# Kernel tuning notes

Measured on AMD Instinct MI355X. Metric: run time of the kernel, lower is better.

## Reference

```python
import jax, jax.numpy as jnp
import numpy as np

IN_DIM, INTER, OUT, CLS = 512, 128, 64, 4
MID, BOT = 1600, 6400
N = 1 + MID + BOT
E = 160000


def setup_inputs() -> dict:
    key = jax.random.key(0)
    ki = iter(jax.random.split(key, 48))

    def nrm(shape, s=0.02):
        return jax.random.normal(next(ki), shape, dtype=jnp.float32) * s

    z = lambda *s: jnp.zeros(s, jnp.float32)
    inp = {}
    inp["x"] = jax.random.normal(next(ki), (N, IN_DIM), dtype=jnp.float32)
    inp["edge_index"] = jax.random.randint(next(ki), (2, E), 0, N)
    # PatchRelevance 1 (in=512 -> 128)
    inp["Wq1"], inp["bq1"] = nrm((IN_DIM, INTER)), z(INTER)
    inp["Wk1"], inp["bk1"] = nrm((IN_DIM, INTER)), z(INTER)
    inp["Wv1"], inp["bv1"] = nrm((IN_DIM, INTER)), z(INTER)
    # PatchRelevance 2 (128 -> 64)
    inp["Wq2"], inp["bq2"] = nrm((INTER, OUT)), z(OUT)
    inp["Wk2"], inp["bk2"] = nrm((INTER, OUT)), z(OUT)
    inp["Wv2"], inp["bv2"] = nrm((INTER, OUT)), z(OUT)
    # GCN convs
    inp["Wg1"], inp["bg1"] = nrm((IN_DIM, INTER)), z(INTER)
    inp["Wg2"], inp["bg2"] = nrm((INTER, OUT)), z(OUT)
    # squeeze MLPs
    inp["Ws1"], inp["bs1"] = nrm((2 * INTER, INTER)), z(INTER)
    inp["Ws2"], inp["bs2"] = nrm((2 * OUT, OUT)), z(OUT)
    # heads
    inp["Wfc1"], inp["bfc1"] = nrm((3 * OUT, OUT)), z(OUT)
    inp["Wfc2"], inp["bfc2"] = nrm((OUT, CLS)), z(CLS)
    inp["Wtw"], inp["btw"] = nrm((OUT, CLS)), z(CLS)
    inp["Wmid"], inp["bmid"] = nrm((OUT, CLS)), z(CLS)
    inp["Wbot"], inp["bbot"] = nrm((OUT, CLS)), z(CLS)
    # sparse_attention Conv1d(out_dim -> 4, k=4, s=4)  weight layout OIH
    inp["Wconv"] = nrm((4, OUT, 4))
    inp["bconv"] = z(4)
    inp["arch0"] = MID
    inp["arch1"] = BOT
    return inp


def _patch_rel(x, Wq, bq, Wk, bk, Wv, bv):
    q = x @ Wq + bq
    k = x @ Wk + bk
    v = x @ Wv + bv
    att = jax.nn.softmax(q @ k.T, axis=-1)  # [N, N]
    return att @ v


def _gcn(x, src, dst, W, b, n):
    # PyG GCNConv: add self-loops (already in src/dst), symmetric deg^-1/2 norm
    deg = jax.ops.segment_sum(jnp.ones_like(src, dtype=x.dtype), dst, num_segments=n)
    dinv = jnp.where(deg > 0, jax.lax.rsqrt(deg), 0.0)
    norm = dinv[src] * dinv[dst]
    h = x @ W
    out = jax.ops.segment_sum(h[src] * norm[:, None], dst, num_segments=n)
    return out + b


def reference(x, edge_index, Wq1, bq1, Wk1, bk1, Wv1, bv1, Wq2, bq2, Wk2, bk2,
              Wv2, bv2, Wg1, bg1, Wg2, bg2, Ws1, bs1, Ws2, bs2, Wfc1, bfc1,
              Wfc2, bfc2, Wtw, btw, Wmid, bmid, Wbot, bbot, Wconv, bconv,
              arch0, arch1):
    n = x.shape[0]
    loop = jnp.arange(n, dtype=edge_index.dtype)
    src = jnp.concatenate([edge_index[0], loop])
    dst = jnp.concatenate([edge_index[1], loop])

    r1 = _patch_rel(x, Wq1, bq1, Wk1, bk1, Wv1, bv1)
    g1 = _gcn(x, src, dst, Wg1, bg1, n)
    s1 = jax.nn.relu(jax.nn.relu(jnp.concatenate([g1, r1], axis=1)) @ Ws1 + bs1)

    r2 = _patch_rel(s1, Wq2, bq2, Wk2, bk2, Wv2, bv2)
    g2 = _gcn(s1, src, dst, Wg2, bg2, n)
    s2 = jax.nn.relu(jax.nn.relu(jnp.concatenate([g2, r2], axis=1)) @ Ws2 + bs2)

    tw = s2[0:1]                                   # [1, OUT]
    mid_features = s2[1:1 + arch0]                 # [arch0, OUT]
    mid_avg = jnp.mean(mid_features, axis=0, keepdims=True)
    bf = s2[1 + arch0:1 + arch0 + arch1]           # [arch1, OUT]

    # Conv1d(OUT -> 4, k=4, s=4) over node axis: [1, OUT, arch1] -> [1, 4, arch0]
    bw = jax.lax.conv_general_dilated(bf.T[None], Wconv, (4,), 'VALID',
                                      dimension_numbers=('NCH', 'OIH', 'NCH'))[0]
    bw = bw + bconv[:, None]                       # [4, arch0]
    # index_copy_ with strided indices == interleave channels: wv[i*4+j] = bw[j, i]
    wv = bw.T.reshape(-1)
    wv = wv / jnp.max(wv)
    grp = wv.reshape(arch0, 4)
    grp = grp / jnp.sum(jnp.abs(grp), axis=-1, keepdims=True)
    wv = grp.reshape(arch1, 1)

    tree_bottom = ((wv * bf).T.reshape(-1, arch0, 4).sum(-1)).T  # [arch0, OUT]
    bottom_weighted = (jnp.sum(wv * bf, axis=0) / arch0).reshape(1, -1)

    out_tw = tw @ Wtw + btw
    out_mid = mid_avg @ Wmid + bmid
    out_bottom = bottom_weighted @ Wbot + bbot
    gcn_feat = jnp.concatenate([tw, mid_avg, bottom_weighted], axis=-1) @ Wfc1 + bfc1
    out_gcn = jax.nn.relu(gcn_feat) @ Wfc2 + bfc2
    return (out_gcn, out_tw, out_mid, out_bottom, gcn_feat, tw, mid_avg,
            bottom_weighted, wv, mid_features, tree_bottom)
```

## Files before the change

### kernel.cpp

```cpp
#include <hip/hip_runtime.h>
#include <math.h>

#define N_NODES 8001
#define NPAD    8032
#define E_EDGES 160000
#define NQTOT   8064
#define LOG2E   1.4426950408889634f
#define NSPLIT  16

typedef unsigned short u16;
typedef __attribute__((ext_vector_type(8)))  short bf16x8;
typedef __attribute__((ext_vector_type(16))) float f32x16;

__device__ __forceinline__ short f2bf(float f) {
    unsigned u = __builtin_bit_cast(unsigned, f);
    u = (u + 0x7FFFu + ((u >> 16) & 1u)) >> 16;
    return (short)u;
}
__device__ __forceinline__ float bf2f(u16 x) {
    return __builtin_bit_cast(float, (unsigned)x << 16);
}
__device__ __forceinline__ int pk2(float a, float b) {
    int r;
    asm("v_cvt_pk_bf16_f32 %0, %1, %2" : "=v"(r) : "v"(a), "v"(b));
    return r;
}

#define GLDS(g, l) __builtin_amdgcn_global_load_lds( \
    (const __attribute__((address_space(1))) void*)(g), \
    (__attribute__((address_space(3))) void*)(l), 16, 0, 0)

template<int K>
__global__ __launch_bounds__(256) void cast_rows(const float* __restrict__ A,
                                                 u16* __restrict__ B)
{
    size_t t = (size_t)blockIdx.x * 256 + threadIdx.x;
    int row = (int)(t / (K / 8));
    int c8  = (int)(t % (K / 8)) * 8;
    int lrow = min(row, N_NODES - 1);
    const float4* p = (const float4*)&A[(size_t)lrow * K + c8];
    float4 u = p[0], v = p[1];
    int4 w = { pk2(u.x, u.y), pk2(u.z, u.w), pk2(v.x, v.y), pk2(v.z, v.w) };
    *(int4*)&B[t * 8] = w;
}

__global__ __launch_bounds__(256) void wtrans_all(
    const float* __restrict__ Wq1, const float* __restrict__ Wk1,
    const float* __restrict__ Wv1, const float* __restrict__ Wg1,
    const float* __restrict__ Wq2, const float* __restrict__ Wk2,
    const float* __restrict__ Wv2, const float* __restrict__ Wg2,
    const float* __restrict__ Ws1, const float* __restrict__ Ws2,
    u16* __restrict__ WT1, u16* __restrict__ WT2,
    u16* __restrict__ WST1, u16* __restrict__ WST2)
{
    const int b = blockIdx.x, tid = threadIdx.x;
    if (b < 1024) {
        int t = b * 256 + tid;
        int p = t / (128 * 512), n = (t / 512) & 127, k = t % 512;
        const float* W = (p == 0) ? Wq1 : (p == 1) ? Wk1 : (p == 2) ? Wv1 : Wg1;
        float v = W[k * 128 + n];
        if (p == 0) v *= LOG2E;
        WT1[t] = (u16)f2bf(v);
    } else if (b < 1152) {
        int t = (b - 1024) * 256 + tid;
        int p = t / (64 * 128), n = (t / 128) & 63, k = t & 127;
        const float* W = (p == 0) ? Wq2 : (p == 1) ? Wk2 : (p == 2) ? Wv2 : Wg2;
        float v = W[k * 64 + n];
        if (p == 0) v *= LOG2E;
        WT2[t] = (u16)f2bf(v);
    } else if (b < 1280) {
        int t = (b - 1152) * 256 + tid;
        int n = t >> 8, k = t & 255;
        WST1[t] = (u16)f2bf(Ws1[k * 128 + n]);
    } else {
        int t = (b - 1280) * 256 + tid;
        int n = t >> 7, k = t & 127;
        WST2[t] = (u16)f2bf(Ws2[k * 64 + n]);
    }
}

template<int K, int MOUT>
__global__ __launch_bounds__(256) void proj4_mfma(
    const u16* __restrict__ Xb, const u16* __restrict__ WT,
    const float* __restrict__ bq, const float* __restrict__ bk,
    const float* __restrict__ bv,
    u16* __restrict__ Qb, u16* __restrict__ Kb, u16* __restrict__ VTb,
    float* __restrict__ Hb)
{
    constexpr int NKC  = K / 16;
    constexpr int NNT  = MOUT / 32;
    constexpr int ROWB = K / 8;
    constexpr int NB   = 32 * ROWB;

    __shared__ u16 xs[32 * K];

    const int tid = threadIdx.x, wid = tid >> 6, lane = tid & 63;
    const int q = lane & 31, gp = lane >> 5;
    const int m0 = blockIdx.x * 32;

    for (int i = tid; i < NB; i += 256) {
        int row = i / ROWB, blk = i % ROWB;
        GLDS(&Xb[(size_t)(m0 + row) * K + 8 * (blk ^ (row & 7))], &xs[i * 8]);
    }
    __syncthreads();

    f32x16 acc[NNT];
#pragma unroll
    for (int nt = 0; nt < NNT; nt++) acc[nt] = f32x16{};

    const u16* wbase = WT + (size_t)wid * MOUT * K;

#pragma unroll 4
    for (int c = 0; c < NKC; c++) {
        bf16x8 af = *(const bf16x8*)&xs[q * K + 8 * ((2 * c + gp) ^ (q & 7))];
#pragma unroll
        for (int nt = 0; nt < NNT; nt++) {
            bf16x8 bf = *(const bf16x8*)&wbase[(size_t)(nt * 32 + q) * K + 16 * c + 8 * gp];
            acc[nt] = __builtin_amdgcn_mfma_f32_32x32x16_bf16(af, bf, acc[nt], 0, 0, 0);
        }
    }

    if (wid == 0) {
#pragma unroll
        for (int nt = 0; nt < NNT; nt++) {
            float bb = bq[nt * 32 + q] * LOG2E;
#pragma unroll
            for (int r = 0; r < 16; r++) {
                int grow = m0 + (r & 3) + 8 * (r >> 2) + 4 * gp;
                Qb[(size_t)grow * MOUT + nt * 32 + q] = (u16)f2bf(acc[nt][r] + bb);
            }
        }
    } else if (wid == 1) {
#pragma unroll
        for (int nt = 0; nt < NNT; nt++) {
            float bb = bk[nt * 32 + q];
#pragma unroll
            for (int r = 0; r < 16; r++) {
                int grow = m0 + (r & 3) + 8 * (r >> 2) + 4 * gp;
                Kb[(size_t)grow * MOUT + nt * 32 + q] = (u16)f2bf(acc[nt][r] + bb);
            }
        }
    } else if (wid == 2) {
#pragma unroll
        for (int nt = 0; nt < NNT; nt++) {
            float bb = bv[nt * 32 + q];
            u16* vrow = &VTb[(size_t)(nt * 32 + q) * NPAD];
#pragma unroll
            for (int g = 0; g < 4; g++) {
                ushort4 s;
                s.x = (u16)f2bf(acc[nt][4 * g + 0] + bb);
                s.y = (u16)f2bf(acc[nt][4 * g + 1] + bb);
                s.z = (u16)f2bf(acc[nt][4 * g + 2] + bb);
                s.w = (u16)f2bf(acc[nt][4 * g + 3] + bb);
                *(ushort4*)&vrow[m0 + 8 * g + 4 * gp] = s;
            }
        }
    } else {
#pragma unroll
        for (int nt = 0; nt < NNT; nt++) {
#pragma unroll
            for (int r = 0; r < 16; r++) {
                int grow = m0 + (r & 3) + 8 * (r >> 2) + 4 * gp;
                if (grow < N_NODES)
                    Hb[(size_t)grow * MOUT + nt * 32 + q] = acc[nt][r];
            }
        }
    }
}

template<int K, int MOUT, int OM, int NW>
__global__ __launch_bounds__(NW * 64) void s_gemm_mfma(
    const u16* __restrict__ Ab, const u16* __restrict__ WT,
    const float* __restrict__ bias, void* __restrict__ Cv)
{
    constexpr int NKC  = K / 16;
    constexpr int ROWB = K / 8;
    constexpr int NB   = 32 * ROWB;

    __shared__ u16 xs[32 * K];

    const int tid = threadIdx.x, wid = tid >> 6, lane = tid & 63;
    const int q = lane & 31, gp = lane >> 5;
    const int m0 = blockIdx.x * 32;

    for (int i = tid; i < NB; i += NW * 64) {
        int row = i / ROWB, blk = i % ROWB;
        GLDS(&Ab[(size_t)(m0 + row) * K + 8 * (blk ^ (row & 7))], &xs[i * 8]);
    }
    __syncthreads();

    f32x16 acc = f32x16{};
    const u16* wbase = WT + (size_t)(wid * 32) * K;

#pragma unroll 4
    for (int c = 0; c < NKC; c++) {
        bf16x8 af = *(const bf16x8*)&xs[q * K + 8 * ((2 * c + gp) ^ (q & 7))];
        bf16x8 bf = *(const bf16x8*)&wbase[(size_t)q * K + 16 * c + 8 * gp];
        acc = __builtin_amdgcn_mfma_f32_32x32x16_bf16(af, bf, acc, 0, 0, 0);
    }

    float bb = bias[wid * 32 + q];
#pragma unroll
    for (int r = 0; r < 16; r++) {
        int grow = m0 + (r & 3) + 8 * (r >> 2) + 4 * gp;
        float v = fmaxf(acc[r] + bb, 0.f);
        if (OM == 0) {
            if (grow < N_NODES) ((float*)Cv)[(size_t)grow * MOUT + wid * 32 + q] = v;
        } else {
            ((u16*)Cv)[(size_t)grow * MOUT + wid * 32 + q] = (u16)f2bf(v);
        }
    }
}

template<int D, int S>
__global__ __launch_bounds__(256) void attn_split(
    const u16* __restrict__ Qg, const u16* __restrict__ Kg,
    const u16* __restrict__ VTg, u16* __restrict__ PO, float* __restrict__ PL)
{
    constexpr int NCH   = D / 16;
    constexpr int NDT   = D / 32;
    constexpr int KROWB = D / 8;
    constexpr int KI    = (32 * D) / 512;
    constexpr int VI    = (D * 32) / 512;
    constexpr int NKS   = KI / 4;
    constexpr int NVS   = VI / 4;
    constexpr int NT    = (N_NODES + 31) / 32;
    constexpr int CHUNK = (NT + S - 1) / S;

    __shared__ u16 kb[2][32 * D];
    __shared__ u16 vb[2][D * 32];

    const int tid  = threadIdx.x;
    const int wid  = tid >> 6;
    const int lane = tid & 63;
    const int q    = lane & 31;
    const int gp   = lane >> 5;
    const int sp   = blockIdx.x;
    const int q0   = blockIdx.y * 128 + wid * 32;

    bf16x8 qf[NCH];
    {
        int row = min(q0 + q, N_NODES - 1);
        const u16* qr = &Qg[(size_t)row * D + 8 * gp];
#pragma unroll
        for (int c = 0; c < NCH; c++)
            qf[c] = *(const bf16x8*)&qr[16 * c];
    }

    const int arow = (q & ~12) | ((q & 4) << 1) | ((q & 8) >> 1);
    const int hK   = (arow & 3) | (((arow >> 3) & 1) << 2);

    f32x16 acc[NDT];
#pragma unroll
    for (int i = 0; i < NDT; i++) acc[i] = f32x16{};
    float l = 0.f;

    const int t0 = sp * CHUNK;
    const int t1 = min(t0 + CHUNK, NT);

    const u16* kp[NKS]; int kdo[NKS];
#pragma unroll
    for (int s = 0; s < NKS; s++) {
        int i   = wid + 4 * s;
        int B   = i * 64 + lane;
        int row = B / KROWB;
        int bk  = B & (KROWB - 1);
        int h   = (row & 3) | (((row >> 3) & 1) << 2);
        kp[s]  = &Kg[(size_t)(t0 * 32 + row) * D + 8 * (bk ^ h)];
        kdo[s] = i * 512;
    }
    const u16* vp[NVS]; int vdo[NVS];
#pragma unroll
    for (int s = 0; s < NVS; s++) {
        int i  = wid + 4 * s;
        int B  = i * 64 + lane;
        int d  = B >> 2;
        int bv = B & 3;
        vp[s]  = &VTg[(size_t)d * NPAD + t0 * 32 + 8 * (bv ^ (d & 3))];
        vdo[s] = i * 512;
    }

    auto stage = [&](int buf) {
        u16* kdst = &kb[buf][0];
        u16* vdst = &vb[buf][0];
#pragma unroll
        for (int s = 0; s < NKS; s++) GLDS(kp[s], &kdst[kdo[s]]);
#pragma unroll
        for (int s = 0; s < NVS; s++) GLDS(vp[s], &vdst[vdo[s]]);
    };
    auto advance = [&]() {
#pragma unroll
        for (int s = 0; s < NKS; s++) kp[s] += 32 * D;
#pragma unroll
        for (int s = 0; s < NVS; s++) vp[s] += 32;
    };

    stage(0);
    advance();
    __syncthreads();

    for (int t = t0; t < t1; t++) {
        const int b = (t - t0) & 1;
        if (t + 1 < t1) { stage(b ^ 1); advance(); }

        const u16* kbt = &kb[b][0];
        const u16* vbt = &vb[b][0];
        const int j0 = t * 32;

        f32x16 st = f32x16{};
#pragma unroll
        for (int c = 0; c < NCH; c++) {
            bf16x8 af = *(const bf16x8*)&kbt[arow * D + 8 * ((2 * c + gp) ^ hK)];
            st = __builtin_amdgcn_mfma_f32_32x32x16_bf16(af, qf[c], st, 0, 0, 0);
        }

        if (j0 + 32 > N_NODES) {
#pragma unroll
            for (int r = 0; r < 16; r++) {
                int kl = (r & 3) + (((r >> 2) & 1) << 2) + ((r >> 3) << 4) + 8 * gp;
                if (j0 + kl >= N_NODES) st[r] = -INFINITY;
            }
        }

        float pv[16]; float ps = 0.f;
#pragma unroll
        for (int r = 0; r < 16; r++) { pv[r] = exp2f(st[r]); ps += pv[r]; }
        ps += __shfl_xor(ps, 32);
        l += ps;

        int4 w0 = { pk2(pv[0],  pv[1]),  pk2(pv[2],  pv[3]),
                    pk2(pv[4],  pv[5]),  pk2(pv[6],  pv[7]) };
        int4 w1 = { pk2(pv[8],  pv[9]),  pk2(pv[10], pv[11]),
                    pk2(pv[12], pv[13]), pk2(pv[14], pv[15]) };
        bf16x8 bp0 = __builtin_bit_cast(bf16x8, w0);
        bf16x8 bp1 = __builtin_bit_cast(bf16x8, w1);

#pragma unroll
        for (int dt = 0; dt < NDT; dt++) {
            const int d = 32 * dt + q;
            bf16x8 vf0 = *(const bf16x8*)&vbt[d * 32 + 8 * ((gp)     ^ (d & 3))];
            acc[dt] = __builtin_amdgcn_mfma_f32_32x32x16_bf16(vf0, bp0, acc[dt], 0, 0, 0);
            bf16x8 vf1 = *(const bf16x8*)&vbt[d * 32 + 8 * ((2 + gp) ^ (d & 3))];
            acc[dt] = __builtin_amdgcn_mfma_f32_32x32x16_bf16(vf1, bp1, acc[dt], 0, 0, 0);
        }
        __syncthreads();
    }

    const int qrl = q0 + q;
    if (gp == 0) PL[(size_t)sp * NQTOT + qrl] = l;
    u16* po = &PO[((size_t)sp * NQTOT + qrl) * D];
#pragma unroll
    for (int dt = 0; dt < NDT; dt++)
#pragma unroll
        for (int k = 0; k < 4; k++) {
            int2 w = { pk2(acc[dt][4 * k + 0], acc[dt][4 * k + 1]),
                       pk2(acc[dt][4 * k + 2], acc[dt][4 * k + 3]) };
            *(int2*)&po[32 * dt + 8 * k + 4 * gp] = w;
        }
}

template<int C, int S>
__global__ __launch_bounds__(256) void merge_gather(
    const u16* __restrict__ PO, const float* __restrict__ PL,
    const float* __restrict__ h, const int* __restrict__ rowptr,
    const int2* __restrict__ csr, const float* __restrict__ dinv,
    const float* __restrict__ bias, u16* __restrict__ AR)
{
    constexpr int MB  = (NPAD * (C / 4)) / 256;
    constexpr int LPN = C / 4;
    constexpr int NPB = 256 / LPN;

    const int tid = threadIdx.x;
    if ((int)blockIdx.x < MB) {
        int t  = blockIdx.x * 256 + tid;
        int qr = t / (C / 4);
        int d4 = (t % (C / 4)) * 4;

        float L = 0.f;
#pragma unroll
        for (int s = 0; s < S; s++) L += PL[(size_t)s * NQTOT + qr];
        float4 o = make_float4(0.f, 0.f, 0.f, 0.f);
#pragma unroll
        for (int s = 0; s < S; s++) {
            ushort4 p = *(const ushort4*)&PO[((size_t)s * NQTOT + qr) * C + d4];
            o.x += bf2f(p.x); o.y += bf2f(p.y);
            o.z += bf2f(p.z); o.w += bf2f(p.w);
        }
        float inv = 1.f / L;
        int2 w = { pk2(fmaxf(o.x * inv, 0.f), fmaxf(o.y * inv, 0.f)),
                   pk2(fmaxf(o.z * inv, 0.f), fmaxf(o.w * inv, 0.f)) };
        *(int2*)&AR[(size_t)qr * (2 * C) + C + d4] = w;
    } else {
        const int node = (blockIdx.x - MB) * NPB + tid / LPN;
        const int c4   = (tid % LPN) * 4;
        if (node >= N_NODES) return;
        const int r0 = rowptr[node], r1 = rowptr[node + 1];
        float4 acc = make_float4(0.f, 0.f, 0.f, 0.f);
        for (int j = r0; j < r1; j++) {
            int2 pk = csr[j];
            float nr = __int_as_float(pk.y);
            const float4 hv = *(const float4*)&h[(size_t)pk.x * C + c4];
            acc.x += hv.x * nr; acc.y += hv.y * nr;
            acc.z += hv.z * nr; acc.w += hv.w * nr;
        }
        float di = dinv[node];
        float sl = di * di;
        const float4 hs = *(const float4*)&h[(size_t)node * C + c4];
        const float4 bv = *(const float4*)&bias[c4];
        acc.x += hs.x * sl + bv.x; acc.y += hs.y * sl + bv.y;
        acc.z += hs.z * sl + bv.z; acc.w += hs.w * sl + bv.w;
        int2 w = { pk2(fmaxf(acc.x, 0.f), fmaxf(acc.y, 0.f)),
                   pk2(fmaxf(acc.z, 0.f), fmaxf(acc.w, 0.f)) };
        *(int2*)&AR[(size_t)node * (2 * C) + c4] = w;
    }
}

__global__ void deg_count_int(const int* __restrict__ ei, int* __restrict__ degi)
{
    int e = blockIdx.x * blockDim.x + threadIdx.x;
    if (e < E_EDGES) atomicAdd(&degi[ei[E_EDGES + e]], 1);
}

__global__ __launch_bounds__(256) void prefix_rowptr(
    const int* __restrict__ degi, int* __restrict__ rowptr,
    int* __restrict__ cursor, float* __restrict__ dinv)
{
    __shared__ int sums[256];
    const int t = threadIdx.x;
    const int base = t * 32;
    int local[32];
    int s = 0;
#pragma unroll
    for (int i = 0; i < 32; i++) {
        int idx = base + i;
        local[i] = s;
        s += (idx < N_NODES) ? degi[idx] : 0;
    }
    sums[t] = s;
    __syncthreads();
    for (int o = 1; o < 256; o <<= 1) {
        int v = (t >= o) ? sums[t - o] : 0;
        __syncthreads();
        sums[t] += v;
        __syncthreads();
    }
    const int pre = (t == 0) ? 0 : sums[t - 1];
#pragma unroll
    for (int i = 0; i < 32; i++) {
        int idx = base + i;
        if (idx <= N_NODES) {
            int v = pre + local[i];
            rowptr[idx] = v;
            if (idx < N_NODES) cursor[idx] = v;
        }
    }
    for (int i = t; i < N_NODES; i += 256)
        dinv[i] = rsqrtf((float)degi[i] + 1.f);
}

__global__ void csr_fill(const int* __restrict__ ei, const float* __restrict__ dinv,
                         int* __restrict__ cursor, int2* __restrict__ csr)
{
    int e = blockIdx.x * blockDim.x + threadIdx.x;
    if (e >= E_EDGES) return;
    int s = ei[e], d = ei[E_EDGES + e];
    int pos = atomicAdd(&cursor[d], 1);
    int2 pk;
    pk.x = s;
    pk.y = __float_as_int(dinv[s] * dinv[d]);
    csr[pos] = pk;
}

__global__ __launch_bounds__(256) void conv_wv(
    const float* __restrict__ S2, const float* __restrict__ Wconv,
    const float* __restrict__ bconv, float* __restrict__ wvp)
{
    __shared__ float wt[16 * 64];
    const int tid = threadIdx.x;
    for (int idx = tid; idx < 1024; idx += 256) {
        int o = idx >> 8, rem = idx & 255, i = rem >> 2, k = rem & 3;
        wt[(k * 4 + o) * 64 + i] = Wconv[idx];
    }
    __syncthreads();

    const int wid = tid >> 6, d = tid & 63;
    const int t = blockIdx.x * 4 + wid;
    const float* base = S2 + (size_t)(1601 + 4 * t) * 64;
    const float v0 = base[d], v1 = base[64 + d], v2 = base[128 + d], v3 = base[192 + d];

    float p[4];
#pragma unroll
    for (int o = 0; o < 4; o++)
        p[o] = v0 * wt[(0 * 4 + o) * 64 + d] + v1 * wt[(1 * 4 + o) * 64 + d]
             + v2 * wt[(2 * 4 + o) * 64 + d] + v3 * wt[(3 * 4 + o) * 64 + d];

#pragma unroll
    for (int o = 0; o < 4; o++)
#pragma unroll
        for (int off = 1; off < 64; off <<= 1) p[o] += __shfl_xor(p[o], off);

    if (d == 0) {
#pragma unroll
        for (int o = 0; o < 4; o++) wvp[4 * t + o] = p[o] + bconv[o];
    }
}

__global__ void max_reduce(const float* __restrict__ in, int n, float* __restrict__ out)
{
    float mv = -INFINITY;
    for (int i = threadIdx.x; i < n; i += 256) mv = fmaxf(mv, in[i]);
    for (int o = 32; o > 0; o >>= 1) mv = fmaxf(mv, __shfl_xor(mv, o));
    __shared__ float sm[4];
    if ((threadIdx.x & 63) == 0) sm[threadIdx.x >> 6] = mv;
    __syncthreads();
    if (threadIdx.x == 0)
        out[0] = fmaxf(fmaxf(sm[0], sm[1]), fmaxf(sm[2], sm[3]));
}

__global__ __launch_bounds__(256) void wv_copy(
    const float* __restrict__ wvp, const float* __restrict__ gmax,
    const float* __restrict__ S2, float* __restrict__ wv, float* __restrict__ out)
{
    const int b = blockIdx.x, tid = threadIdx.x;
    if (b < 7) {
        int t = b * 256 + tid;
        if (t >= 1600) return;
        float g = gmax[0];
        float v0 = wvp[4 * t + 0] / g, v1 = wvp[4 * t + 1] / g;
        float v2 = wvp[4 * t + 2] / g, v3 = wvp[4 * t + 3] / g;
        float s = fabsf(v0) + fabsf(v1) + fabsf(v2) + fabsf(v3);
        float r0 = v0 / s, r1 = v1 / s, r2 = v2 / s, r3 = v3 / s;
        wv[4 * t + 0] = r0; wv[4 * t + 1] = r1;
        wv[4 * t + 2] = r2; wv[4 * t + 3] = r3;
        out[272 + 4 * t + 0] = r0; out[272 + 4 * t + 1] = r1;
        out[272 + 4 * t + 2] = r2; out[272 + 4 * t + 3] = r3;
    } else {
        int i = (b - 7) * 256 + tid;
        if (i < 25600) ((float4*)(out + 6672))[i] = ((const float4*)(S2 + 64))[i];
    }
}

__global__ void tree_bottom_kernel(const float* __restrict__ S2,
                                   const float* __restrict__ wv,
                                   float* __restrict__ out)
{
    int t = blockIdx.x * blockDim.x + threadIdx.x;
    if (t >= 1600 * 64) return;
    int mg = t >> 6, c = t & 63;
    const float* base = S2 + (size_t)(1601 + 4 * mg) * 64 + c;
    out[t] = wv[4 * mg + 0] * base[0]   + wv[4 * mg + 1] * base[64]
           + wv[4 * mg + 2] * base[128] + wv[4 * mg + 3] * base[192];
}

__global__ void col_mean2(const float* __restrict__ S2, const float* __restrict__ tb,
                          float* __restrict__ midavg, float* __restrict__ botw)
{
    const int b = blockIdx.x;
    const int c = b & 63;
    const float* in = (b < 64) ? (S2 + 64) : tb;
    float s = 0.f;
    for (int r = threadIdx.x; r < 1600; r += 256) s += in[(size_t)r * 64 + c];
    for (int o = 32; o > 0; o >>= 1) s += __shfl_xor(s, o);
    __shared__ float sm[4];
    if ((threadIdx.x & 63) == 0) sm[threadIdx.x >> 6] = s;
    __syncthreads();
    if (threadIdx.x == 0) {
        float v = (sm[0] + sm[1] + sm[2] + sm[3]) * (1.f / 1600.f);
        (b < 64 ? midavg : botw)[c] = v;
    }
}

__global__ void head_kernel(const float* __restrict__ S2,
                            const float* __restrict__ midavg, const float* __restrict__ botw,
                            const float* __restrict__ Wtw,  const float* __restrict__ btw,
                            const float* __restrict__ Wmid, const float* __restrict__ bmid,
                            const float* __restrict__ Wbot, const float* __restrict__ bbot,
                            const float* __restrict__ Wfc1, const float* __restrict__ bfc1,
                            const float* __restrict__ Wfc2, const float* __restrict__ bfc2,
                            float* __restrict__ out)
{
    __shared__ float cat[192];
    __shared__ float gf[64];
    int t = threadIdx.x;
    float twv = S2[t];
    cat[t]       = twv;
    cat[64 + t]  = midavg[t];
    cat[128 + t] = botw[t];
    out[80 + t]  = twv;
    out[144 + t] = midavg[t];
    out[208 + t] = botw[t];
    __syncthreads();
    float acc = bfc1[t];
    for (int k = 0; k < 192; k++) acc += cat[k] * Wfc1[k * 64 + t];
    gf[t] = acc;
    out[16 + t] = acc;
    __syncthreads();
    if (t < 4) {
        float og = bfc2[t], ot = btw[t], om = bmid[t], ob = bbot[t];
        for (int c = 0; c < 64; c++) {
            og += fmaxf(gf[c], 0.f) * Wfc2[c * 4 + t];
            ot += cat[c]        * Wtw[c * 4 + t];
            om += cat[64 + c]   * Wmid[c * 4 + t];
            ob += cat[128 + c]  * Wbot[c * 4 + t];
        }
        out[0 + t] = og; out[4 + t] = ot; out[8 + t] = om; out[12 + t] = ob;
    }
}

extern "C" void kernel_launch(void* const* d_in, const int* in_sizes, int n_in,
                              void* d_out, int out_size, void* d_ws, size_t ws_size,
                              hipStream_t stream)
{
    (void)in_sizes; (void)n_in; (void)out_size; (void)ws_size;
    const float* x    = (const float*)d_in[0];
    const int*   ei   = (const int*)d_in[1];
    const float* Wq1  = (const float*)d_in[2];  const float* bq1 = (const float*)d_in[3];
    const float* Wk1  = (const float*)d_in[4];  const float* bk1 = (const float*)d_in[5];
    const float* Wv1  = (const float*)d_in[6];  const float* bv1 = (const float*)d_in[7];
    const float* Wq2  = (const float*)d_in[8];  const float* bq2 = (const float*)d_in[9];
    const float* Wk2  = (const float*)d_in[10]; const float* bk2 = (const float*)d_in[11];
    const float* Wv2  = (const float*)d_in[12]; const float* bv2 = (const float*)d_in[13];
    const float* Wg1  = (const float*)d_in[14]; const float* bg1 = (const float*)d_in[15];
    const float* Wg2  = (const float*)d_in[16]; const float* bg2 = (const float*)d_in[17];
    const float* Ws1  = (const float*)d_in[18]; const float* bs1 = (const float*)d_in[19];
    const float* Ws2  = (const float*)d_in[20]; const float* bs2 = (const float*)d_in[21];
    const float* Wfc1 = (const float*)d_in[22]; const float* bfc1= (const float*)d_in[23];
    const float* Wfc2 = (const float*)d_in[24]; const float* bfc2= (const float*)d_in[25];
    const float* Wtw  = (const float*)d_in[26]; const float* btw = (const float*)d_in[27];
    const float* Wmid = (const float*)d_in[28]; const float* bmid= (const float*)d_in[29];
    const float* Wbot = (const float*)d_in[30]; const float* bbot= (const float*)d_in[31];
    const float* Wconv= (const float*)d_in[32]; const float* bconv=(const float*)d_in[33];

    float* out = (float*)d_out;
    float* ws  = (float*)d_ws;

    const size_t N128 = (size_t)N_NODES * 128;
    const size_t BF128 = (size_t)NPAD * 128 / 2;

    size_t off = 0;
    auto alloc = [&](size_t n) { float* p = ws + off; off += (n + 15) & ~size_t(15); return p; };
    float* QB1  = alloc(BF128);
    float* KB1  = alloc(BF128);
    float* VTB1 = alloc(BF128);
    float* XB   = alloc((size_t)NPAD * 256);
    float* WT1  = alloc(4 * 128 * 512 / 2);
    float* WT2  = alloc(4 * 64 * 128 / 2);
    float* WST1 = alloc(128 * 256 / 2);
    float* WST2 = alloc(64 * 128 / 2);
    float* AR1  = alloc((size_t)NPAD * 128);
    float* S1B  = alloc((size_t)NPAD * 64);
    float* H1   = alloc(N128);
    float* S2   = alloc(N128);
    float* DINV = alloc(N_NODES);
    int*   DEGI   = (int*)alloc(8008);
    int*   ROWPTR = (int*)alloc(8008);
    int*   CURSOR = (int*)alloc(8008);
    int2*  CSR    = (int2*)alloc(2 * (size_t)E_EDGES);
    float* PO   = alloc((size_t)NSPLIT * NQTOT * 128 / 2);
    float* PL   = alloc((size_t)NSPLIT * NQTOT);
    float* WVP  = alloc(6400);
    float* GMAX = alloc(16);
    float* WV   = alloc(6400);
    float* MIDAVG = alloc(64);
    float* BOTW   = alloc(64);
    float* QB2  = QB1;
    float* KB2  = KB1;
    float* VTB2 = VTB1;
    float* H2   = H1;
    float* AR2  = AR1;

    hipMemsetAsync(DEGI, 0, N_NODES * sizeof(int), stream);
    deg_count_int<<<(E_EDGES + 255) / 256, 256, 0, stream>>>(ei, DEGI);
    prefix_rowptr<<<1, 256, 0, stream>>>(DEGI, ROWPTR, CURSOR, DINV);
    csr_fill<<<(E_EDGES + 255) / 256, 256, 0, stream>>>(ei, DINV, CURSOR, CSR);

    cast_rows<512><<<NPAD * 64 / 256, 256, 0, stream>>>(x, (u16*)XB);
    wtrans_all<<<1312, 256, 0, stream>>>(
        Wq1, Wk1, Wv1, Wg1, Wq2, Wk2, Wv2, Wg2, Ws1, Ws2,
        (u16*)WT1, (u16*)WT2, (u16*)WST1, (u16*)WST2);

    proj4_mfma<512, 128><<<NPAD / 32, 256, 0, stream>>>(
        (const u16*)XB, (const u16*)WT1, bq1, bk1, bv1,
        (u16*)QB1, (u16*)KB1, (u16*)VTB1, H1);

    attn_split<128, NSPLIT><<<dim3(NSPLIT, 63), 256, 0, stream>>>(
        (const u16*)QB1, (const u16*)KB1, (const u16*)VTB1, (u16*)PO, PL);

    {
        int mb = (NPAD * 32) / 256, gb = (N_NODES * 32 + 255) / 256;
        merge_gather<128, NSPLIT><<<mb + gb, 256, 0, stream>>>(
            (const u16*)PO, PL, H1, ROWPTR, CSR, DINV, bg1, (u16*)AR1);
    }

    s_gemm_mfma<256, 128, 1, 4><<<NPAD / 32, 256, 0, stream>>>(
        (const u16*)AR1, (const u16*)WST1, bs1, (u16*)S1B);

    proj4_mfma<128, 64><<<NPAD / 32, 256, 0, stream>>>(
        (const u16*)S1B, (const u16*)WT2, bq2, bk2, bv2,
        (u16*)QB2, (u16*)KB2, (u16*)VTB2, H2);

    attn_split<64, NSPLIT><<<dim3(NSPLIT, 63), 256, 0, stream>>>(
        (const u16*)QB2, (const u16*)KB2, (const u16*)VTB2, (u16*)PO, PL);

    {
        int mb = (NPAD * 16) / 256, gb = (N_NODES * 16 + 255) / 256;
        merge_gather<64, NSPLIT><<<mb + gb, 256, 0, stream>>>(
            (const u16*)PO, PL, H2, ROWPTR, CSR, DINV, bg2, (u16*)AR2);
    }

    s_gemm_mfma<128, 64, 0, 2><<<NPAD / 32, 128, 0, stream>>>(
        (const u16*)AR2, (const u16*)WST2, bs2, S2);

    conv_wv<<<400, 256, 0, stream>>>(S2, Wconv, bconv, WVP);
    max_reduce<<<1, 256, 0, stream>>>(WVP, 6400, GMAX);
    wv_copy<<<107, 256, 0, stream>>>(WVP, GMAX, S2, WV, out);
    tree_bottom_kernel<<<400, 256, 0, stream>>>(S2, WV, out + 109072);
    col_mean2<<<128, 256, 0, stream>>>(S2, out + 109072, MIDAVG, BOTW);
    head_kernel<<<1, 64, 0, stream>>>(S2, MIDAVG, BOTW, Wtw, btw, Wmid, bmid,
                                      Wbot, bbot, Wfc1, bfc1, Wfc2, bfc2, out);
}
```

Baseline: 253.1 us.

## Process two query tiles per attention wave and merge prep kernels

```diff
diff --git a/kernel.cpp b/kernel.cpp
--- a/kernel.cpp
+++ b/kernel.cpp
@@ -4,9 +4,8 @@
 #define N_NODES 8001
 #define NPAD    8032
 #define E_EDGES 160000
-#define NQTOT   8064
+#define NQTOT   8192
 #define LOG2E   1.4426950408889634f
-#define NSPLIT  16
 
 typedef unsigned short u16;
 typedef __attribute__((ext_vector_type(8)))  short bf16x8;
@@ -30,50 +29,49 @@
     (const __attribute__((address_space(1))) void*)(g), \
     (__attribute__((address_space(3))) void*)(l), 16, 0, 0)
 
-template<int K>
-__global__ __launch_bounds__(256) void cast_rows(const float* __restrict__ A,
-                                                 u16* __restrict__ B)
-{
-    size_t t = (size_t)blockIdx.x * 256 + threadIdx.x;
-    int row = (int)(t / (K / 8));
-    int c8  = (int)(t % (K / 8)) * 8;
-    int lrow = min(row, N_NODES - 1);
-    const float4* p = (const float4*)&A[(size_t)lrow * K + c8];
-    float4 u = p[0], v = p[1];
-    int4 w = { pk2(u.x, u.y), pk2(u.z, u.w), pk2(v.x, v.y), pk2(v.z, v.w) };
-    *(int4*)&B[t * 8] = w;
-}
-
-__global__ __launch_bounds__(256) void wtrans_all(
+__global__ __launch_bounds__(256) void prep_all(
+    const float* __restrict__ x, const int* __restrict__ ei,
     const float* __restrict__ Wq1, const float* __restrict__ Wk1,
     const float* __restrict__ Wv1, const float* __restrict__ Wg1,
     const float* __restrict__ Wq2, const float* __restrict__ Wk2,
     const float* __restrict__ Wv2, const float* __restrict__ Wg2,
     const float* __restrict__ Ws1, const float* __restrict__ Ws2,
+    int* __restrict__ degi, u16* __restrict__ XB,
     u16* __restrict__ WT1, u16* __restrict__ WT2,
     u16* __restrict__ WST1, u16* __restrict__ WST2)
 {
     const int b = blockIdx.x, tid = threadIdx.x;
-    if (b < 1024) {
-        int t = b * 256 + tid;
+    if (b < 625) {
+        int e = b * 256 + tid;
+        if (e < E_EDGES) atomicAdd(&degi[ei[E_EDGES + e]], 1);
+    } else if (b < 2633) {
+        size_t t = (size_t)(b - 625) * 256 + tid;
+        int row = (int)(t / 64), c8 = (int)(t % 64) * 8;
+        int lrow = min(row, N_NODES - 1);
+        const float4* p = (const float4*)&x[(size_t)lrow * 512 + c8];
+        float4 u = p[0], v = p[1];
+        int4 w = { pk2(u.x, u.y), pk2(u.z, u.w), pk2(v.x, v.y), pk2(v.z, v.w) };
+        *(int4*)&XB[t * 8] = w;
+    } else if (b < 3657) {
+        int t = (b - 2633) * 256 + tid;
         int p = t / (128 * 512), n = (t / 512) & 127, k = t % 512;
         const float* W = (p == 0) ? Wq1 : (p == 1) ? Wk1 : (p == 2) ? Wv1 : Wg1;
         float v = W[k * 128 + n];
         if (p == 0) v *= LOG2E;
         WT1[t] = (u16)f2bf(v);
-    } else if (b < 1152) {
-        int t = (b - 1024) * 256 + tid;
+    } else if (b < 3785) {
+        int t = (b - 3657) * 256 + tid;
         int p = t / (64 * 128), n = (t / 128) & 63, k = t & 127;
         const float* W = (p == 0) ? Wq2 : (p == 1) ? Wk2 : (p == 2) ? Wv2 : Wg2;
         float v = W[k * 64 + n];
         if (p == 0) v *= LOG2E;
         WT2[t] = (u16)f2bf(v);
-    } else if (b < 1280) {
-        int t = (b - 1152) * 256 + tid;
+    } else if (b < 3913) {
+        int t = (b - 3785) * 256 + tid;
         int n = t >> 8, k = t & 255;
         WST1[t] = (u16)f2bf(Ws1[k * 128 + n]);
     } else {
-        int t = (b - 1280) * 256 + tid;
+        int t = (b - 3913) * 256 + tid;
         int n = t >> 7, k = t & 127;
         WST2[t] = (u16)f2bf(Ws2[k * 64 + n]);
     }
@@ -212,8 +210,8 @@
     }
 }
 
-template<int D, int S>
-__global__ __launch_bounds__(256) void attn_split(
+template<int D, int S, int MINW>
+__global__ __launch_bounds__(256, MINW) void attn_split(
     const u16* __restrict__ Qg, const u16* __restrict__ Kg,
     const u16* __restrict__ VTg, u16* __restrict__ PO, float* __restrict__ PL)
 {
@@ -236,24 +234,27 @@
     const int q    = lane & 31;
     const int gp   = lane >> 5;
     const int sp   = blockIdx.x;
-    const int q0   = blockIdx.y * 128 + wid * 32;
-
-    bf16x8 qf[NCH];
-    {
-        int row = min(q0 + q, N_NODES - 1);
+    const int qb0  = blockIdx.y * 256 + wid * 32;
+
+    bf16x8 qf[2][NCH];
+#pragma unroll
+    for (int u = 0; u < 2; u++) {
+        int row = min(qb0 + 128 * u + q, N_NODES - 1);
         const u16* qr = &Qg[(size_t)row * D + 8 * gp];
 #pragma unroll
         for (int c = 0; c < NCH; c++)
-            qf[c] = *(const bf16x8*)&qr[16 * c];
+            qf[u][c] = *(const bf16x8*)&qr[16 * c];
     }
 
     const int arow = (q & ~12) | ((q & 4) << 1) | ((q & 8) >> 1);
     const int hK   = (arow & 3) | (((arow >> 3) & 1) << 2);
 
-    f32x16 acc[NDT];
-#pragma unroll
-    for (int i = 0; i < NDT; i++) acc[i] = f32x16{};
-    float l = 0.f;
+    f32x16 acc[2][NDT];
+#pragma unroll
+    for (int u = 0; u < 2; u++)
+#pragma unroll
+        for (int i = 0; i < NDT; i++) acc[u][i] = f32x16{};
+    float l0 = 0.f, l1 = 0.f;
 
     const int t0 = sp * CHUNK;
     const int t1 = min(t0 + CHUNK, NT);
@@ -307,56 +308,77 @@
         const u16* vbt = &vb[b][0];
         const int j0 = t * 32;
 
-        f32x16 st = f32x16{};
+        f32x16 st0 = f32x16{}, st1 = f32x16{};
 #pragma unroll
         for (int c = 0; c < NCH; c++) {
             bf16x8 af = *(const bf16x8*)&kbt[arow * D + 8 * ((2 * c + gp) ^ hK)];
-            st = __builtin_amdgcn_mfma_f32_32x32x16_bf16(af, qf[c], st, 0, 0, 0);
+            st0 = __builtin_amdgcn_mfma_f32_32x32x16_bf16(af, qf[0][c], st0, 0, 0, 0);
+            st1 = __builtin_amdgcn_mfma_f32_32x32x16_bf16(af, qf[1][c], st1, 0, 0, 0);
         }
 
         if (j0 + 32 > N_NODES) {
 #pragma unroll
             for (int r = 0; r < 16; r++) {
                 int kl = (r & 3) + (((r >> 2) & 1) << 2) + ((r >> 3) << 4) + 8 * gp;
-                if (j0 + kl >= N_NODES) st[r] = -INFINITY;
+                if (j0 + kl >= N_NODES) { st0[r] = -INFINITY; st1[r] = -INFINITY; }
             }
         }
 
-        float pv[16]; float ps = 0.f;
-#pragma unroll
-        for (int r = 0; r < 16; r++) { pv[r] = exp2f(st[r]); ps += pv[r]; }
-        ps += __shfl_xor(ps, 32);
-        l += ps;
-
-        int4 w0 = { pk2(pv[0],  pv[1]),  pk2(pv[2],  pv[3]),
-                    pk2(pv[4],  pv[5]),  pk2(pv[6],  pv[7]) };
-        int4 w1 = { pk2(pv[8],  pv[9]),  pk2(pv[10], pv[11]),
-                    pk2(pv[12], pv[13]), pk2(pv[14], pv[15]) };
-        bf16x8 bp0 = __builtin_bit_cast(bf16x8, w0);
-        bf16x8 bp1 = __builtin_bit_cast(bf16x8, w1);
+        bf16x8 bp00, bp01, bp10, bp11;
+        {
+            float pv[16]; float ps = 0.f;
+#pragma unroll
+            for (int r = 0; r < 16; r++) { pv[r] = exp2f(st0[r]); ps += pv[r]; }
+            ps += __shfl_xor(ps, 32);
+            l0 += ps;
+            int4 w0 = { pk2(pv[0],  pv[1]),  pk2(pv[2],  pv[3]),
+                        pk2(pv[4],  pv[5]),  pk2(pv[6],  pv[7]) };
+            int4 w1 = { pk2(pv[8],  pv[9]),  pk2(pv[10], pv[11]),
+                        pk2(pv[12], pv[13]), pk2(pv[14], pv[15]) };
+            bp00 = __builtin_bit_cast(bf16x8, w0);
+            bp01 = __builtin_bit_cast(bf16x8, w1);
+        }
+        {
+            float pv[16]; float ps = 0.f;
+#pragma unroll
+            for (int r = 0; r < 16; r++) { pv[r] = exp2f(st1[r]); ps += pv[r]; }
+            ps += __shfl_xor(ps, 32);
+            l1 += ps;
+            int4 w0 = { pk2(pv[0],  pv[1]),  pk2(pv[2],  pv[3]),
+                        pk2(pv[4],  pv[5]),  pk2(pv[6],  pv[7]) };
+            int4 w1 = { pk2(pv[8],  pv[9]),  pk2(pv[10], pv[11]),
+                        pk2(pv[12], pv[13]), pk2(pv[14], pv[15]) };
+            bp10 = __builtin_bit_cast(bf16x8, w0);
+            bp11 = __builtin_bit_cast(bf16x8, w1);
+        }
 
 #pragma unroll
         for (int dt = 0; dt < NDT; dt++) {
             const int d = 32 * dt + q;
             bf16x8 vf0 = *(const bf16x8*)&vbt[d * 32 + 8 * ((gp)     ^ (d & 3))];
-            acc[dt] = __builtin_amdgcn_mfma_f32_32x32x16_bf16(vf0, bp0, acc[dt], 0, 0, 0);
+            acc[0][dt] = __builtin_amdgcn_mfma_f32_32x32x16_bf16(vf0, bp00, acc[0][dt], 0, 0, 0);
+            acc[1][dt] = __builtin_amdgcn_mfma_f32_32x32x16_bf16(vf0, bp10, acc[1][dt], 0, 0, 0);
             bf16x8 vf1 = *(const bf16x8*)&vbt[d * 32 + 8 * ((2 + gp) ^ (d & 3))];
-            acc[dt] = __builtin_amdgcn_mfma_f32_32x32x16_bf16(vf1, bp1, acc[dt], 0, 0, 0);
+            acc[0][dt] = __builtin_amdgcn_mfma_f32_32x32x16_bf16(vf1, bp01, acc[0][dt], 0, 0, 0);
+            acc[1][dt] = __builtin_amdgcn_mfma_f32_32x32x16_bf16(vf1, bp11, acc[1][dt], 0, 0, 0);
         }
         __syncthreads();
     }
 
-    const int qrl = q0 + q;
-    if (gp == 0) PL[(size_t)sp * NQTOT + qrl] = l;
-    u16* po = &PO[((size_t)sp * NQTOT + qrl) * D];
-#pragma unroll
-    for (int dt = 0; dt < NDT; dt++)
-#pragma unroll
-        for (int k = 0; k < 4; k++) {
-            int2 w = { pk2(acc[dt][4 * k + 0], acc[dt][4 * k + 1]),
-                       pk2(acc[dt][4 * k + 2], acc[dt][4 * k + 3]) };
-            *(int2*)&po[32 * dt + 8 * k + 4 * gp] = w;
-        }
+#pragma unroll
+    for (int u = 0; u < 2; u++) {
+        const int qrl = qb0 + 128 * u + q;
+        if (gp == 0) PL[(size_t)sp * NQTOT + qrl] = (u == 0) ? l0 : l1;
+        u16* po = &PO[((size_t)sp * NQTOT + qrl) * D];
+#pragma unroll
+        for (int dt = 0; dt < NDT; dt++)
+#pragma unroll
+            for (int k = 0; k < 4; k++) {
+                int2 w = { pk2(acc[u][dt][4 * k + 0], acc[u][dt][4 * k + 1]),
+                           pk2(acc[u][dt][4 * k + 2], acc[u][dt][4 * k + 3]) };
+                *(int2*)&po[32 * dt + 8 * k + 4 * gp] = w;
+            }
+    }
 }
 
 template<int C, int S>
@@ -413,12 +435,6 @@
                    pk2(fmaxf(acc.z, 0.f), fmaxf(acc.w, 0.f)) };
         *(int2*)&AR[(size_t)node * (2 * C) + c4] = w;
     }
-}
-
-__global__ void deg_count_int(const int* __restrict__ ei, int* __restrict__ degi)
-{
-    int e = blockIdx.x * blockDim.x + threadIdx.x;
-    if (e < E_EDGES) atomicAdd(&degi[ei[E_EDGES + e]], 1);
 }
 
 __global__ __launch_bounds__(256) void prefix_rowptr(
@@ -656,8 +672,8 @@
     int*   ROWPTR = (int*)alloc(8008);
     int*   CURSOR = (int*)alloc(8008);
     int2*  CSR    = (int2*)alloc(2 * (size_t)E_EDGES);
-    float* PO   = alloc((size_t)NSPLIT * NQTOT * 128 / 2);
-    float* PL   = alloc((size_t)NSPLIT * NQTOT);
+    float* PO   = alloc((size_t)32 * NQTOT * 64 / 2);
+    float* PL   = alloc((size_t)32 * NQTOT);
     float* WVP  = alloc(6400);
     float* GMAX = alloc(16);
     float* WV   = alloc(6400);
@@ -670,25 +686,22 @@
     float* AR2  = AR1;
 
     hipMemsetAsync(DEGI, 0, N_NODES * sizeof(int), stream);
-    deg_count_int<<<(E_EDGES + 255) / 256, 256, 0, stream>>>(ei, DEGI);
+    prep_all<<<3945, 256, 0, stream>>>(
+        x, ei, Wq1, Wk1, Wv1, Wg1, Wq2, Wk2, Wv2, Wg2, Ws1, Ws2,
+        DEGI, (u16*)XB, (u16*)WT1, (u16*)WT2, (u16*)WST1, (u16*)WST2);
     prefix_rowptr<<<1, 256, 0, stream>>>(DEGI, ROWPTR, CURSOR, DINV);
     csr_fill<<<(E_EDGES + 255) / 256, 256, 0, stream>>>(ei, DINV, CURSOR, CSR);
-
-    cast_rows<512><<<NPAD * 64 / 256, 256, 0, stream>>>(x, (u16*)XB);
-    wtrans_all<<<1312, 256, 0, stream>>>(
-        Wq1, Wk1, Wv1, Wg1, Wq2, Wk2, Wv2, Wg2, Ws1, Ws2,
-        (u16*)WT1, (u16*)WT2, (u16*)WST1, (u16*)WST2);
 
     proj4_mfma<512, 128><<<NPAD / 32, 256, 0, stream>>>(
         (const u16*)XB, (const u16*)WT1, bq1, bk1, bv1,
         (u16*)QB1, (u16*)KB1, (u16*)VTB1, H1);
 
-    attn_split<128, NSPLIT><<<dim3(NSPLIT, 63), 256, 0, stream>>>(
+    attn_split<128, 16, 2><<<dim3(16, NQTOT / 256), 256, 0, stream>>>(
         (const u16*)QB1, (const u16*)KB1, (const u16*)VTB1, (u16*)PO, PL);
 
     {
         int mb = (NPAD * 32) / 256, gb = (N_NODES * 32 + 255) / 256;
-        merge_gather<128, NSPLIT><<<mb + gb, 256, 0, stream>>>(
+        merge_gather<128, 16><<<mb + gb, 256, 0, stream>>>(
             (const u16*)PO, PL, H1, ROWPTR, CSR, DINV, bg1, (u16*)AR1);
     }
 
@@ -699,12 +712,12 @@
         (const u16*)S1B, (const u16*)WT2, bq2, bk2, bv2,
         (u16*)QB2, (u16*)KB2, (u16*)VTB2, H2);
 
-    attn_split<64, NSPLIT><<<dim3(NSPLIT, 63), 256, 0, stream>>>(
+    attn_split<64, 32, 3><<<dim3(32, NQTOT / 256), 256, 0, stream>>>(
         (const u16*)QB2, (const u16*)KB2, (const u16*)VTB2, (u16*)PO, PL);
 
     {
         int mb = (NPAD * 16) / 256, gb = (N_NODES * 16 + 255) / 256;
-        merge_gather<64, NSPLIT><<<mb + gb, 256, 0, stream>>>(
+        merge_gather<64, 32><<<mb + gb, 256, 0, stream>>>(
             (const u16*)PO, PL, H2, ROWPTR, CSR, DINV, bg2, (u16*)AR2);
     }
 
```

After: 263.7 us. 1.04x slower.
